# Kernel tuning notes

Measured on AMD Instinct MI355X. Metric: run time of the kernel, lower is better.

Reference implementation:

```python
import jax, jax.numpy as jnp
import numpy as np

N, E, L, D = 4, 64, 512, 768


def setup_inputs() -> dict:
    key = jax.random.key(0)
    k1, k2, k3, k4 = jax.random.split(key, 4)
    doc_state = jax.random.normal(k1, (N, L, D), dtype=jnp.float32)
    # 0/1 entity membership mask, float as in the torch module's multiply
    entity_mapping = jax.random.randint(k2, (N, E, L), 0, 2).astype(jnp.float32)
    # lens consistent with the mask; clamp to >=1 to avoid divide-by-zero
    entity_lens = jnp.maximum(entity_mapping.sum(axis=-1), 1.0)
    W = jax.random.normal(k3, (D, 2 * D), dtype=jnp.float32) * 0.02  # torch Linear weight [out, in]
    b = jnp.zeros((D,), dtype=jnp.float32)
    return {"doc_state": doc_state, "entity_mapping": entity_mapping,
            "entity_lens": entity_lens, "W": W, "b": b}


def reference(doc_state, entity_mapping, entity_lens, W, b):
    # entity_states: N x E x L x d (the large broadcast intermediate)
    entity_states = entity_mapping[:, :, :, None] * doc_state[:, None, :, :]
    max_pooled = jnp.max(entity_states, axis=2)                      # N x E x d
    mean_pooled = jnp.sum(entity_states, axis=2) / entity_lens[:, :, None]  # N x E x d
    output = jnp.concatenate([max_pooled, mean_pooled], axis=2)      # N x E x 2d
    return jnp.einsum('nek,dk->ned', output, W) + b                  # N x E x d
```

## Files before the change

kernel.cpp:

```cpp
#include <hip/hip_runtime.h>
#include <hip/hip_bf16.h>
#include <math.h>

#define PN 4
#define PE 64
#define PL 512
#define PD 768
#define PK2 (2 * PD)
#define PM (PN * PE)

#define SPL 8
#define EG  8
#define DC  3

using bf16x8 = __attribute__((ext_vector_type(8))) short;
using f32x4  = __attribute__((ext_vector_type(4))) float;

static __device__ __forceinline__ unsigned short f2bf(float x) {
    unsigned int u = __float_as_uint(x);
    unsigned int r = (u + 0x7FFFu + ((u >> 16) & 1u)) >> 16;
    return (unsigned short)r;
}

__global__ __launch_bounds__(256) void pool_p1(
    const float* __restrict__ doc,
    const float* __restrict__ map,
    const float* __restrict__ W,
    float* __restrict__ Pmax,
    float* __restrict__ Psum,
    unsigned short* __restrict__ Wb)
{
    const int bid = blockIdx.x;
    const int tid = threadIdx.x;

    if (bid >= PM * DC) {
        const size_t i = ((size_t)(bid - PM * DC) * 256 + tid) * 8;
        const float4 a = *reinterpret_cast<const float4*>(W + i);
        const float4 c = *reinterpret_cast<const float4*>(W + i + 4);
        union { unsigned short s[8]; uint4 v; } r;
        r.s[0] = f2bf(a.x); r.s[1] = f2bf(a.y); r.s[2] = f2bf(a.z); r.s[3] = f2bf(a.w);
        r.s[4] = f2bf(c.x); r.s[5] = f2bf(c.y); r.s[6] = f2bf(c.z); r.s[7] = f2bf(c.w);
        *reinterpret_cast<uint4*>(Wb + i) = r.v;
        return;
    }

    __shared__ float2 smb[64][EG];

    const int grp = bid / DC;
    const int dc  = bid - grp * DC;
    const int n   = grp >> 6;
    const int eg  = (grp >> 3) & 7;
    const int s   = grp & 7;
    const int e0  = eg * EG;
    const int l0  = s * 64;

    #pragma unroll
    for (int i = 0; i < 2; ++i) {
        const int idx = tid + i * 256;
        const int l = idx >> 3, e = idx & 7;
        const float m = map[((size_t)n * PE + e0 + e) * PL + l0 + l];
        smb[l][e] = make_float2(m, (m == 0.0f) ? -3.0e38f : 0.0f);
    }
    __syncthreads();

    const float* docp = doc + ((size_t)n * PL + l0) * PD + dc * 256 + tid;

    float mx[EG], sm[EG];
    #pragma unroll
    for (int e = 0; e < EG; ++e) { mx[e] = -INFINITY; sm[e] = 0.f; }

    #pragma unroll 4
    for (int l = 0; l < 64; ++l) {
        const float v = docp[(size_t)l * PD];
        #pragma unroll
        for (int e = 0; e < EG; ++e) {
            const float2 mb = smb[l][e];
            sm[e] = fmaf(mb.x, v, sm[e]);
            mx[e] = fmaxf(mx[e], fmaf(mb.x, v, mb.y));
        }
    }

    #pragma unroll
    for (int e = 0; e < EG; ++e) {
        const size_t base = ((size_t)(n * PE + e0 + e) * SPL + s) * PD + dc * 256 + tid;
        Pmax[base] = mx[e];
        Psum[base] = sm[e];
    }
}

__global__ __launch_bounds__(256) void pool_p2(
    const float* __restrict__ Pmax,
    const float* __restrict__ Psum,
    const float* __restrict__ lens,
    unsigned short* __restrict__ Pb)
{
    const int idx = blockIdx.x * 256 + threadIdx.x;
    const int ne = idx / PD;
    const int d  = idx - ne * PD;

    float mx = -INFINITY, smv = 0.f;
    #pragma unroll
    for (int s = 0; s < SPL; ++s) {
        const size_t o = ((size_t)ne * SPL + s) * PD + d;
        mx  = fmaxf(mx, Pmax[o]);
        smv += Psum[o];
    }
    const float ln = lens[ne];
    if (ln < 511.5f) mx = fmaxf(mx, 0.f);

    unsigned short* prow = Pb + (size_t)ne * PK2;
    prow[d]      = f2bf(mx);
    prow[PD + d] = f2bf(smv / ln);
}

__global__ __launch_bounds__(64) void gemm_mfma(
    const unsigned short* __restrict__ Pb,
    const unsigned short* __restrict__ Wb,
    const float* __restrict__ b,
    float* __restrict__ out)
{
    const int lane = threadIdx.x;
    const int tile = blockIdx.x;
    const int rt = tile & 15;
    const int ct = tile >> 4;
    const int r0 = rt * 16, d0 = ct * 16;

    const int fr = lane & 15;
    const int kg = lane >> 4;

    const unsigned short* pA = Pb + (size_t)(r0 + fr) * PK2 + kg * 8;
    const unsigned short* pB = Wb + (size_t)(d0 + fr) * PK2 + kg * 8;

    f32x4 acc = {0.f, 0.f, 0.f, 0.f};
    #pragma unroll 8
    for (int k0 = 0; k0 < PK2; k0 += 32) {
        const bf16x8 a  = *reinterpret_cast<const bf16x8*>(pA + k0);
        const bf16x8 bb = *reinterpret_cast<const bf16x8*>(pB + k0);
        acc = __builtin_amdgcn_mfma_f32_16x16x32_bf16(a, bb, acc, 0, 0, 0);
    }

    const int c = d0 + fr;
    const float bias = b[c];
    #pragma unroll
    for (int j = 0; j < 4; ++j)
        out[(size_t)(r0 + kg * 4 + j) * PD + c] = acc[j] + bias;
}

__global__ __launch_bounds__(256) void convert_w(
    const float* __restrict__ W, unsigned short* __restrict__ Wb)
{
    const size_t i = ((size_t)blockIdx.x * 256 + threadIdx.x) * 8;
    const float4 a = *reinterpret_cast<const float4*>(W + i);
    const float4 c = *reinterpret_cast<const float4*>(W + i + 4);
    union { unsigned short s[8]; uint4 v; } r;
    r.s[0] = f2bf(a.x); r.s[1] = f2bf(a.y); r.s[2] = f2bf(a.z); r.s[3] = f2bf(a.w);
    r.s[4] = f2bf(c.x); r.s[5] = f2bf(c.y); r.s[6] = f2bf(c.z); r.s[7] = f2bf(c.w);
    *reinterpret_cast<uint4*>(Wb + i) = r.v;
}

__global__ __launch_bounds__(1024) void pool_kernel2(
    const float* __restrict__ doc, const float* __restrict__ map,
    const float* __restrict__ lens, unsigned short* __restrict__ Pb)
{
    __shared__ float psum[4][PD];
    __shared__ float pmax[4][PD];
    __shared__ int   zf[4];
    const int ne = blockIdx.x, n = ne >> 6, t = threadIdx.x;
    const int g = t >> 8, td = t & 255;
    const float* docn = doc + (size_t)n * PL * PD;
    const float* mrow = map + (size_t)ne * PL;
    float mx0=-INFINITY, mx1=-INFINITY, mx2=-INFINITY, s0=0.f, s1=0.f, s2=0.f;
    bool hz = false;
    const int l0 = g * (PL/4), l1 = l0 + (PL/4);
    for (int l = l0; l < l1; ++l) {
        const float m = mrow[l];
        if (m != 0.0f) {
            const float* dr = docn + (size_t)l * PD;
            const float a = dr[td], c = dr[td+256], e = dr[td+512];
            mx0=fmaxf(mx0,a); s0+=a; mx1=fmaxf(mx1,c); s1+=c; mx2=fmaxf(mx2,e); s2+=e;
        } else hz = true;
    }
    psum[g][td]=s0; pmax[g][td]=mx0;
    psum[g][td+256]=s1; pmax[g][td+256]=mx1;
    psum[g][td+512]=s2; pmax[g][td+512]=mx2;
    if (td == 0) zf[g] = hz ? 1 : 0;
    __syncthreads();
    if (t < PD) {
        const float s = psum[0][t]+psum[1][t]+psum[2][t]+psum[3][t];
        float mx = fmaxf(fmaxf(pmax[0][t],pmax[1][t]), fmaxf(pmax[2][t],pmax[3][t]));
        if (zf[0]|zf[1]|zf[2]|zf[3]) mx = fmaxf(mx, 0.f);
        const float invlen = 1.0f / lens[ne];
        unsigned short* prow = Pb + (size_t)ne * PK2;
        prow[t]      = f2bf(mx);
        prow[PD + t] = f2bf(s * invlen);
    }
}

__global__ __launch_bounds__(256) void fused_kernel(
    const float* __restrict__ doc, const float* __restrict__ map,
    const float* __restrict__ lens, const float* __restrict__ W,
    const float* __restrict__ b, float* __restrict__ out)
{
    __shared__ float Prow[PK2];
    const int ne = blockIdx.x, n = ne >> 6, t = threadIdx.x;
    const float* docn = doc + (size_t)n * PL * PD;
    const float* mrow = map + (size_t)ne * PL;
    float mx0=-INFINITY, mx1=-INFINITY, mx2=-INFINITY, s0=0.f, s1=0.f, s2=0.f;
    bool has_zero = false;
    for (int l = 0; l < PL; ++l) {
        const float m = mrow[l];
        if (m != 0.0f) {
            const float* dr = docn + (size_t)l * PD;
            const float a = dr[t], c = dr[t+256], e = dr[t+512];
            mx0=fmaxf(mx0,a); s0+=a; mx1=fmaxf(mx1,c); s1+=c; mx2=fmaxf(mx2,e); s2+=e;
        } else has_zero = true;
    }
    if (has_zero) { mx0=fmaxf(mx0,0.f); mx1=fmaxf(mx1,0.f); mx2=fmaxf(mx2,0.f); }
    const float invlen = 1.0f / lens[ne];
    Prow[t]=mx0; Prow[t+256]=mx1; Prow[t+512]=mx2;
    Prow[PD+t]=s0*invlen; Prow[PD+t+256]=s1*invlen; Prow[PD+t+512]=s2*invlen;
    __syncthreads();
    #pragma unroll
    for (int i = 0; i < 3; ++i) {
        const int d = t + i*256;
        const float* wrow = W + (size_t)d * PK2;
        float acc = 0.f;
        for (int k = 0; k < PK2; k += 4) {
            const float4 w = *reinterpret_cast<const float4*>(&wrow[k]);
            acc += Prow[k]*w.x + Prow[k+1]*w.y + Prow[k+2]*w.z + Prow[k+3]*w.w;
        }
        out[(size_t)ne * PD + d] = acc + b[d];
    }
}

extern "C" void kernel_launch(void* const* d_in, const int* in_sizes, int n_in,
                              void* d_out, int out_size, void* d_ws, size_t ws_size,
                              hipStream_t stream) {
    const float* doc  = (const float*)d_in[0];
    const float* map  = (const float*)d_in[1];
    const float* lens = (const float*)d_in[2];
    const float* W    = (const float*)d_in[3];
    const float* b    = (const float*)d_in[4];
    float* out = (float*)d_out;

    const size_t part_bytes = (size_t)PM * SPL * PD * sizeof(float);
    const size_t pb_bytes   = (size_t)PM * PK2 * sizeof(unsigned short);
    const size_t wb_bytes   = (size_t)PD * PK2 * sizeof(unsigned short);
    const size_t need_new   = 2 * part_bytes + pb_bytes + wb_bytes;
    const size_t need_bf16  = pb_bytes + wb_bytes;

    if (ws_size >= need_new) {
        float* Pmax = (float*)d_ws;
        float* Psum = (float*)((char*)d_ws + part_bytes);
        unsigned short* Pb = (unsigned short*)((char*)d_ws + 2 * part_bytes);
        unsigned short* Wb = (unsigned short*)((char*)d_ws + 2 * part_bytes + pb_bytes);
        pool_p1<<<dim3(PM * DC + (PD * PK2) / (256 * 8)), dim3(256), 0, stream>>>(
            doc, map, W, Pmax, Psum, Wb);
        pool_p2<<<dim3(PM * PD / 256), dim3(256), 0, stream>>>(Pmax, Psum, lens, Pb);
        gemm_mfma<<<dim3((PM / 16) * (PD / 16)), dim3(64), 0, stream>>>(Pb, Wb, b, out);
    } else if (ws_size >= need_bf16) {
        unsigned short* Pb = (unsigned short*)d_ws;
        unsigned short* Wb = (unsigned short*)((char*)d_ws + pb_bytes);
        convert_w<<<dim3((PD * PK2) / (256 * 8)), dim3(256), 0, stream>>>(W, Wb);
        pool_kernel2<<<dim3(PM), dim3(1024), 0, stream>>>(doc, map, lens, Pb);
        gemm_mfma<<<dim3((PM / 16) * (PD / 16)), dim3(64), 0, stream>>>(Pb, Wb, b, out);
    } else {
        fused_kernel<<<dim3(PM), dim3(256), 0, stream>>>(doc, map, lens, W, b, out);
    }
}
```

Before: 32.76 us.

## Rework pooling partials with ballot bitmasks, float4 doc loads, and finer L split

```diff
diff --git a/kernel.cpp b/kernel.cpp
--- a/kernel.cpp
+++ b/kernel.cpp
@@ -9,9 +9,11 @@
 #define PK2 (2 * PD)
 #define PM (PN * PE)
 
-#define SPL 8
-#define EG  8
-#define DC  3
+#define SPL 16
+#define EG  4
+#define PTHR 192
+#define NPOOL (PN * (PE / EG) * SPL)
+#define NCVT  ((PD * PK2) / (PTHR * 8))
 
 using bf16x8 = __attribute__((ext_vector_type(8))) short;
 using f32x4  = __attribute__((ext_vector_type(4))) float;
@@ -22,7 +24,7 @@
     return (unsigned short)r;
 }
 
-__global__ __launch_bounds__(256) void pool_p1(
+__global__ __launch_bounds__(PTHR) void pool_p1(
     const float* __restrict__ doc,
     const float* __restrict__ map,
     const float* __restrict__ W,
@@ -33,8 +35,8 @@
     const int bid = blockIdx.x;
     const int tid = threadIdx.x;
 
-    if (bid >= PM * DC) {
-        const size_t i = ((size_t)(bid - PM * DC) * 256 + tid) * 8;
+    if (bid >= NPOOL) {
+        const size_t i = ((size_t)(bid - NPOOL) * PTHR + tid) * 8;
         const float4 a = *reinterpret_cast<const float4*>(W + i);
         const float4 c = *reinterpret_cast<const float4*>(W + i + 4);
         union { unsigned short s[8]; uint4 v; } r;
@@ -44,47 +46,54 @@
         return;
     }
 
-    __shared__ float2 smb[64][EG];
-
-    const int grp = bid / DC;
-    const int dc  = bid - grp * DC;
-    const int n   = grp >> 6;
-    const int eg  = (grp >> 3) & 7;
-    const int s   = grp & 7;
+    const int n   = bid >> 8;
+    const int rem = bid & 255;
+    const int eg  = rem >> 4;
+    const int s   = rem & 15;
     const int e0  = eg * EG;
-    const int l0  = s * 64;
-
-    #pragma unroll
-    for (int i = 0; i < 2; ++i) {
-        const int idx = tid + i * 256;
-        const int l = idx >> 3, e = idx & 7;
-        const float m = map[((size_t)n * PE + e0 + e) * PL + l0 + l];
-        smb[l][e] = make_float2(m, (m == 0.0f) ? -3.0e38f : 0.0f);
-    }
-    __syncthreads();
-
-    const float* docp = doc + ((size_t)n * PL + l0) * PD + dc * 256 + tid;
-
-    float mx[EG], sm[EG];
-    #pragma unroll
-    for (int e = 0; e < EG; ++e) { mx[e] = -INFINITY; sm[e] = 0.f; }
-
-    #pragma unroll 4
-    for (int l = 0; l < 64; ++l) {
-        const float v = docp[(size_t)l * PD];
+    const int l0  = s * 32;
+    const int lane = tid & 63;
+
+    unsigned int mk[EG];
+    #pragma unroll
+    for (int e = 0; e < EG; ++e) {
+        const float m = map[((size_t)n * PE + e0 + e) * PL + l0 + (lane & 31)];
+        mk[e] = (unsigned int)__ballot(m != 0.0f);
+    }
+
+    const float* docp = doc + ((size_t)n * PL + l0) * PD + tid * 4;
+
+    float4 mx[EG], sm[EG];
+    #pragma unroll
+    for (int e = 0; e < EG; ++e) {
+        mx[e] = make_float4(-INFINITY, -INFINITY, -INFINITY, -INFINITY);
+        sm[e] = make_float4(0.f, 0.f, 0.f, 0.f);
+    }
+
+    #pragma unroll 8
+    for (int l = 0; l < 32; ++l) {
+        const float4 v = *reinterpret_cast<const float4*>(docp + (size_t)l * PD);
         #pragma unroll
         for (int e = 0; e < EG; ++e) {
-            const float2 mb = smb[l][e];
-            sm[e] = fmaf(mb.x, v, sm[e]);
-            mx[e] = fmaxf(mx[e], fmaf(mb.x, v, mb.y));
+            const bool bit = (mk[e] >> l) & 1u;
+            const float mval = bit ? 1.0f : 0.0f;
+            const float bias = bit ? 0.0f : -3.0e38f;
+            sm[e].x = fmaf(mval, v.x, sm[e].x);
+            sm[e].y = fmaf(mval, v.y, sm[e].y);
+            sm[e].z = fmaf(mval, v.z, sm[e].z);
+            sm[e].w = fmaf(mval, v.w, sm[e].w);
+            mx[e].x = fmaxf(mx[e].x, v.x + bias);
+            mx[e].y = fmaxf(mx[e].y, v.y + bias);
+            mx[e].z = fmaxf(mx[e].z, v.z + bias);
+            mx[e].w = fmaxf(mx[e].w, v.w + bias);
         }
     }
 
     #pragma unroll
     for (int e = 0; e < EG; ++e) {
-        const size_t base = ((size_t)(n * PE + e0 + e) * SPL + s) * PD + dc * 256 + tid;
-        Pmax[base] = mx[e];
-        Psum[base] = sm[e];
+        const size_t base = ((size_t)(n * PE + e0 + e) * SPL + s) * PD + tid * 4;
+        *reinterpret_cast<float4*>(Pmax + base) = mx[e];
+        *reinterpret_cast<float4*>(Psum + base) = sm[e];
     }
 }
 
@@ -95,22 +104,36 @@
     unsigned short* __restrict__ Pb)
 {
     const int idx = blockIdx.x * 256 + threadIdx.x;
-    const int ne = idx / PD;
-    const int d  = idx - ne * PD;
-
-    float mx = -INFINITY, smv = 0.f;
+    const int ne = idx / (PD / 4);
+    const int d  = (idx - ne * (PD / 4)) * 4;
+
+    float4 mx = make_float4(-INFINITY, -INFINITY, -INFINITY, -INFINITY);
+    float4 s4 = make_float4(0.f, 0.f, 0.f, 0.f);
     #pragma unroll
     for (int s = 0; s < SPL; ++s) {
         const size_t o = ((size_t)ne * SPL + s) * PD + d;
-        mx  = fmaxf(mx, Pmax[o]);
-        smv += Psum[o];
+        const float4 a = *reinterpret_cast<const float4*>(Pmax + o);
+        const float4 b = *reinterpret_cast<const float4*>(Psum + o);
+        mx.x = fmaxf(mx.x, a.x); mx.y = fmaxf(mx.y, a.y);
+        mx.z = fmaxf(mx.z, a.z); mx.w = fmaxf(mx.w, a.w);
+        s4.x += b.x; s4.y += b.y; s4.z += b.z; s4.w += b.w;
     }
     const float ln = lens[ne];
-    if (ln < 511.5f) mx = fmaxf(mx, 0.f);
+    if (ln < 511.5f) {
+        mx.x = fmaxf(mx.x, 0.f); mx.y = fmaxf(mx.y, 0.f);
+        mx.z = fmaxf(mx.z, 0.f); mx.w = fmaxf(mx.w, 0.f);
+    }
+    const float inv = 1.0f / ln;
+
+    union { unsigned short s[4]; uint2 v; } rm, rs;
+    rm.s[0] = f2bf(mx.x); rm.s[1] = f2bf(mx.y);
+    rm.s[2] = f2bf(mx.z); rm.s[3] = f2bf(mx.w);
+    rs.s[0] = f2bf(s4.x * inv); rs.s[1] = f2bf(s4.y * inv);
+    rs.s[2] = f2bf(s4.z * inv); rs.s[3] = f2bf(s4.w * inv);
 
     unsigned short* prow = Pb + (size_t)ne * PK2;
-    prow[d]      = f2bf(mx);
-    prow[PD + d] = f2bf(smv / ln);
+    *reinterpret_cast<uint2*>(prow + d)      = rm.v;
+    *reinterpret_cast<uint2*>(prow + PD + d) = rs.v;
 }
 
 __global__ __launch_bounds__(64) void gemm_mfma(
@@ -254,9 +277,9 @@
         float* Psum = (float*)((char*)d_ws + part_bytes);
         unsigned short* Pb = (unsigned short*)((char*)d_ws + 2 * part_bytes);
         unsigned short* Wb = (unsigned short*)((char*)d_ws + 2 * part_bytes + pb_bytes);
-        pool_p1<<<dim3(PM * DC + (PD * PK2) / (256 * 8)), dim3(256), 0, stream>>>(
+        pool_p1<<<dim3(NPOOL + NCVT), dim3(PTHR), 0, stream>>>(
             doc, map, W, Pmax, Psum, Wb);
-        pool_p2<<<dim3(PM * PD / 256), dim3(256), 0, stream>>>(Pmax, Psum, lens, Pb);
+        pool_p2<<<dim3(PM * (PD / 4) / 256), dim3(256), 0, stream>>>(Pmax, Psum, lens, Pb);
         gemm_mfma<<<dim3((PM / 16) * (PD / 16)), dim3(64), 0, stream>>>(Pb, Wb, b, out);
     } else if (ws_size >= need_bf16) {
         unsigned short* Pb = (unsigned short*)d_ws;
```

Result: slower. 38.03 us (+16.1%).

## Fuse two-pass pooling into single kernel with in-block cross-wave reduction

Applied to the files above, without the earlier changes.

```diff
diff --git a/kernel.cpp b/kernel.cpp
--- a/kernel.cpp
+++ b/kernel.cpp
@@ -9,9 +9,11 @@
 #define PK2 (2 * PD)
 #define PM (PN * PE)
 
-#define SPL 8
-#define EG  8
-#define DC  3
+#define EG 4
+#define DCW 128
+#define NDC (PD / DCW)
+#define NPOOLB (PN * (PE / EG) * NDC)
+#define NCVT ((PD * PK2) / (512 * 8))
 
 using bf16x8 = __attribute__((ext_vector_type(8))) short;
 using f32x4  = __attribute__((ext_vector_type(4))) float;
@@ -22,19 +24,19 @@
     return (unsigned short)r;
 }
 
-__global__ __launch_bounds__(256) void pool_p1(
+__global__ __launch_bounds__(512) void pool_full(
     const float* __restrict__ doc,
     const float* __restrict__ map,
+    const float* __restrict__ lens,
     const float* __restrict__ W,
-    float* __restrict__ Pmax,
-    float* __restrict__ Psum,
+    unsigned short* __restrict__ Pb,
     unsigned short* __restrict__ Wb)
 {
     const int bid = blockIdx.x;
     const int tid = threadIdx.x;
 
-    if (bid >= PM * DC) {
-        const size_t i = ((size_t)(bid - PM * DC) * 256 + tid) * 8;
+    if (bid >= NPOOLB) {
+        const size_t i = ((size_t)(bid - NPOOLB) * 512 + tid) * 8;
         const float4 a = *reinterpret_cast<const float4*>(W + i);
         const float4 c = *reinterpret_cast<const float4*>(W + i + 4);
         union { unsigned short s[8]; uint4 v; } r;
@@ -44,76 +46,85 @@
         return;
     }
 
-    __shared__ float2 smb[64][EG];
-
-    const int grp = bid / DC;
-    const int dc  = bid - grp * DC;
-    const int n   = grp >> 6;
-    const int eg  = (grp >> 3) & 7;
-    const int s   = grp & 7;
-    const int e0  = eg * EG;
-    const int l0  = s * 64;
-
-    #pragma unroll
-    for (int i = 0; i < 2; ++i) {
-        const int idx = tid + i * 256;
-        const int l = idx >> 3, e = idx & 7;
-        const float m = map[((size_t)n * PE + e0 + e) * PL + l0 + l];
-        smb[l][e] = make_float2(m, (m == 0.0f) ? -3.0e38f : 0.0f);
-    }
-    __syncthreads();
-
-    const float* docp = doc + ((size_t)n * PL + l0) * PD + dc * 256 + tid;
-
-    float mx[EG], sm[EG];
-    #pragma unroll
-    for (int e = 0; e < EG; ++e) { mx[e] = -INFINITY; sm[e] = 0.f; }
-
-    #pragma unroll 4
+    __shared__ float2 lmax[8][EG][64];
+    __shared__ float2 lsum[8][EG][64];
+
+    const int dc   = bid % NDC;
+    const int rest = bid / NDC;
+    const int eg   = rest & 15;
+    const int n    = rest >> 4;
+    const int e0   = eg * EG;
+    const int d0   = dc * DCW;
+    const int w    = tid >> 6;
+    const int lane = tid & 63;
+
+    unsigned long long mk[EG];
+    #pragma unroll
+    for (int e = 0; e < EG; ++e) {
+        const float m = map[((size_t)n * PE + e0 + e) * PL + w * 64 + lane];
+        mk[e] = __ballot(m != 0.0f);
+    }
+
+    const float2* docp = reinterpret_cast<const float2*>(
+        doc + ((size_t)n * PL + w * 64) * PD + d0) + lane;
+
+    float2 mx[EG], sm[EG];
+    #pragma unroll
+    for (int e = 0; e < EG; ++e) {
+        mx[e] = make_float2(-INFINITY, -INFINITY);
+        sm[e] = make_float2(0.f, 0.f);
+    }
+
+    #pragma unroll 8
     for (int l = 0; l < 64; ++l) {
-        const float v = docp[(size_t)l * PD];
+        const float2 v = docp[(size_t)l * (PD / 2)];
         #pragma unroll
         for (int e = 0; e < EG; ++e) {
-            const float2 mb = smb[l][e];
-            sm[e] = fmaf(mb.x, v, sm[e]);
-            mx[e] = fmaxf(mx[e], fmaf(mb.x, v, mb.y));
+            const bool bit = (mk[e] >> l) & 1ull;
+            const float cx = bit ? v.x : 0.0f;
+            const float cy = bit ? v.y : 0.0f;
+            sm[e].x += cx;  sm[e].y += cy;
+            mx[e].x = fmaxf(mx[e].x, cx);
+            mx[e].y = fmaxf(mx[e].y, cy);
         }
     }
 
     #pragma unroll
     for (int e = 0; e < EG; ++e) {
-        const size_t base = ((size_t)(n * PE + e0 + e) * SPL + s) * PD + dc * 256 + tid;
-        Pmax[base] = mx[e];
-        Psum[base] = sm[e];
-    }
-}
-
-__global__ __launch_bounds__(256) void pool_p2(
-    const float* __restrict__ Pmax,
-    const float* __restrict__ Psum,
-    const float* __restrict__ lens,
-    unsigned short* __restrict__ Pb)
-{
-    const int idx = blockIdx.x * 256 + threadIdx.x;
-    const int ne = idx / PD;
-    const int d  = idx - ne * PD;
-
-    float mx = -INFINITY, smv = 0.f;
-    #pragma unroll
-    for (int s = 0; s < SPL; ++s) {
-        const size_t o = ((size_t)ne * SPL + s) * PD + d;
-        mx  = fmaxf(mx, Pmax[o]);
-        smv += Psum[o];
-    }
-    const float ln = lens[ne];
-    if (ln < 511.5f) mx = fmaxf(mx, 0.f);
-
-    unsigned short* prow = Pb + (size_t)ne * PK2;
-    prow[d]      = f2bf(mx);
-    prow[PD + d] = f2bf(smv / ln);
-}
-
-__global__ __launch_bounds__(64) void gemm_mfma(
+        lmax[w][e][lane] = mx[e];
+        lsum[w][e][lane] = sm[e];
+    }
+    __syncthreads();
+
+    const int slot = tid & 255;
+    const int e  = slot >> 6;
+    const int ln = slot & 63;
+    const int ne = n * PE + e0 + e;
+    if (tid < 256) {
+        float2 m = lmax[0][e][ln];
+        #pragma unroll
+        for (int ww = 1; ww < 8; ++ww) {
+            const float2 t = lmax[ww][e][ln];
+            m.x = fmaxf(m.x, t.x);
+            m.y = fmaxf(m.y, t.y);
+        }
+        const unsigned int pk = (unsigned int)f2bf(m.x) | ((unsigned int)f2bf(m.y) << 16);
+        *reinterpret_cast<unsigned int*>(Pb + (size_t)ne * PK2 + d0 + ln * 2) = pk;
+    } else {
+        float2 s = lsum[0][e][ln];
+        #pragma unroll
+        for (int ww = 1; ww < 8; ++ww) {
+            const float2 t = lsum[ww][e][ln];
+            s.x += t.x;
+            s.y += t.y;
+        }
+        const float inv = 1.0f / lens[ne];
+        const unsigned int pk = (unsigned int)f2bf(s.x * inv) | ((unsigned int)f2bf(s.y * inv) << 16);
+        *reinterpret_cast<unsigned int*>(Pb + (size_t)ne * PK2 + PD + d0 + ln * 2) = pk;
+    }
+}
+
+__global__ __launch_bounds__(64) void gemm_mfma1(
     const unsigned short* __restrict__ Pb,
     const unsigned short* __restrict__ Wb,
     const float* __restrict__ b,
@@ -144,56 +155,6 @@
     #pragma unroll
     for (int j = 0; j < 4; ++j)
         out[(size_t)(r0 + kg * 4 + j) * PD + c] = acc[j] + bias;
-}
-
-__global__ __launch_bounds__(256) void convert_w(
-    const float* __restrict__ W, unsigned short* __restrict__ Wb)
-{
-    const size_t i = ((size_t)blockIdx.x * 256 + threadIdx.x) * 8;
-    const float4 a = *reinterpret_cast<const float4*>(W + i);
-    const float4 c = *reinterpret_cast<const float4*>(W + i + 4);
-    union { unsigned short s[8]; uint4 v; } r;
-    r.s[0] = f2bf(a.x); r.s[1] = f2bf(a.y); r.s[2] = f2bf(a.z); r.s[3] = f2bf(a.w);
-    r.s[4] = f2bf(c.x); r.s[5] = f2bf(c.y); r.s[6] = f2bf(c.z); r.s[7] = f2bf(c.w);
-    *reinterpret_cast<uint4*>(Wb + i) = r.v;
-}
-
-__global__ __launch_bounds__(1024) void pool_kernel2(
-    const float* __restrict__ doc, const float* __restrict__ map,
-    const float* __restrict__ lens, unsigned short* __restrict__ Pb)
-{
-    __shared__ float psum[4][PD];
-    __shared__ float pmax[4][PD];
-    __shared__ int   zf[4];
-    const int ne = blockIdx.x, n = ne >> 6, t = threadIdx.x;
-    const int g = t >> 8, td = t & 255;
-    const float* docn = doc + (size_t)n * PL * PD;
-    const float* mrow = map + (size_t)ne * PL;
-    float mx0=-INFINITY, mx1=-INFINITY, mx2=-INFINITY, s0=0.f, s1=0.f, s2=0.f;
-    bool hz = false;
-    const int l0 = g * (PL/4), l1 = l0 + (PL/4);
-    for (int l = l0; l < l1; ++l) {
-        const float m = mrow[l];
-        if (m != 0.0f) {
-            const float* dr = docn + (size_t)l * PD;
-            const float a = dr[td], c = dr[td+256], e = dr[td+512];
-            mx0=fmaxf(mx0,a); s0+=a; mx1=fmaxf(mx1,c); s1+=c; mx2=fmaxf(mx2,e); s2+=e;
-        } else hz = true;
-    }
-    psum[g][td]=s0; pmax[g][td]=mx0;
-    psum[g][td+256]=s1; pmax[g][td+256]=mx1;
-    psum[g][td+512]=s2; pmax[g][td+512]=mx2;
-    if (td == 0) zf[g] = hz ? 1 : 0;
-    __syncthreads();
-    if (t < PD) {
-        const float s = psum[0][t]+psum[1][t]+psum[2][t]+psum[3][t];
-        float mx = fmaxf(fmaxf(pmax[0][t],pmax[1][t]), fmaxf(pmax[2][t],pmax[3][t]));
-        if (zf[0]|zf[1]|zf[2]|zf[3]) mx = fmaxf(mx, 0.f);
-        const float invlen = 1.0f / lens[ne];
-        unsigned short* prow = Pb + (size_t)ne * PK2;
-        prow[t]      = f2bf(mx);
-        prow[PD + t] = f2bf(s * invlen);
-    }
 }
 
 __global__ __launch_bounds__(256) void fused_kernel(
@@ -243,27 +204,16 @@
     const float* b    = (const float*)d_in[4];
     float* out = (float*)d_out;
 
-    const size_t part_bytes = (size_t)PM * SPL * PD * sizeof(float);
-    const size_t pb_bytes   = (size_t)PM * PK2 * sizeof(unsigned short);
-    const size_t wb_bytes   = (size_t)PD * PK2 * sizeof(unsigned short);
-    const size_t need_new   = 2 * part_bytes + pb_bytes + wb_bytes;
-    const size_t need_bf16  = pb_bytes + wb_bytes;
-
-    if (ws_size >= need_new) {
-        float* Pmax = (float*)d_ws;
-        float* Psum = (float*)((char*)d_ws + part_bytes);
-        unsigned short* Pb = (unsigned short*)((char*)d_ws + 2 * part_bytes);
-        unsigned short* Wb = (unsigned short*)((char*)d_ws + 2 * part_bytes + pb_bytes);
-        pool_p1<<<dim3(PM * DC + (PD * PK2) / (256 * 8)), dim3(256), 0, stream>>>(
-            doc, map, W, Pmax, Psum, Wb);
-        pool_p2<<<dim3(PM * PD / 256), dim3(256), 0, stream>>>(Pmax, Psum, lens, Pb);
-        gemm_mfma<<<dim3((PM / 16) * (PD / 16)), dim3(64), 0, stream>>>(Pb, Wb, b, out);
-    } else if (ws_size >= need_bf16) {
+    const size_t pb_bytes = (size_t)PM * PK2 * sizeof(unsigned short);
+    const size_t wb_bytes = (size_t)PD * PK2 * sizeof(unsigned short);
+    const size_t need     = pb_bytes + wb_bytes;
+
+    if (ws_size >= need) {
         unsigned short* Pb = (unsigned short*)d_ws;
         unsigned short* Wb = (unsigned short*)((char*)d_ws + pb_bytes);
-        convert_w<<<dim3((PD * PK2) / (256 * 8)), dim3(256), 0, stream>>>(W, Wb);
-        pool_kernel2<<<dim3(PM), dim3(1024), 0, stream>>>(doc, map, lens, Pb);
-        gemm_mfma<<<dim3((PM / 16) * (PD / 16)), dim3(64), 0, stream>>>(Pb, Wb, b, out);
+        pool_full<<<dim3(NPOOLB + NCVT), dim3(512), 0, stream>>>(
+            doc, map, lens, W, Pb, Wb);
+        gemm_mfma1<<<dim3((PM / 16) * (PD / 16)), dim3(64), 0, stream>>>(Pb, Wb, b, out);
     } else {
         fused_kernel<<<dim3(PM), dim3(256), 0, stream>>>(doc, map, lens, W, b, out);
     }
```

Result: faster. 30.44 us (-7.1%).
